# Performance work log

Measured on AMD Instinct MI355X. Metric: run time of the kernel, lower is better.

The kernel has to match this reference:

```python
import jax, jax.numpy as jnp
import numpy as np

LORA_ALPHA = 16.0
MAX_RANK = 32.0
SCALING = LORA_ALPHA / MAX_RANK  # use_rslora=False path


def setup_inputs() -> dict:
    key = jax.random.key(0)
    ks = jax.random.split(key, 9)
    d = 4096
    x = jax.random.normal(ks[0], (4, 2048, d), dtype=jnp.float32)
    W_base = jax.random.normal(ks[1], (d, d), dtype=jnp.float32) / np.sqrt(d)
    A8 = jax.random.normal(ks[2], (8, d), dtype=jnp.float32) / np.sqrt(d)
    B8 = jax.random.normal(ks[3], (d, 8), dtype=jnp.float32) * 0.01
    A16 = jax.random.normal(ks[4], (16, d), dtype=jnp.float32) / np.sqrt(d)
    B16 = jax.random.normal(ks[5], (d, 16), dtype=jnp.float32) * 0.01
    A32 = jax.random.normal(ks[6], (32, d), dtype=jnp.float32) / np.sqrt(d)
    B32 = jax.random.normal(ks[7], (d, 32), dtype=jnp.float32) * 0.01
    alphas = jax.random.normal(ks[8], (3,), dtype=jnp.float32)
    return {"x": x, "W_base": W_base, "A8": A8, "B8": B8, "A16": A16,
            "B16": B16, "A32": A32, "B32": B32, "alphas": alphas}


def reference(x, W_base, A8, B8, A16, B16, A32, B32, alphas):
    # Base layer: y = x @ W_base^T (nn.Linear, no bias)
    base = jnp.einsum('bsd,od->bso', x, W_base)
    adapter = jnp.zeros_like(base)
    for i, (A, B) in enumerate([(A8, B8), (A16, B16), (A32, B32)]):
        # lora_B(lora_A(x)): (x @ A^T) @ B^T, skinny rank-r GEMMs
        low = jnp.einsum('bsd,rd->bsr', x, A)
        out = jnp.einsum('bsr,dr->bsd', low, B)
        adapter = adapter + alphas[i] * out
    return base + adapter * SCALING
```

## Files before the change

kernel.cpp:

```cpp
#include <hip/hip_runtime.h>
#include <hip/hip_bf16.h>


typedef __attribute__((ext_vector_type(8))) short bf16x8;
typedef __attribute__((ext_vector_type(4))) float f32x4;
typedef __attribute__((ext_vector_type(8))) unsigned short u16x8;

#define GLOBAL_LOAD_LDS16(gp, lp)                                                   \
  __builtin_amdgcn_global_load_lds(                                                 \
      (const __attribute__((address_space(1))) unsigned int*)(gp),                  \
      (__attribute__((address_space(3))) unsigned int*)(lp), 16, 0, 0)

__device__ inline unsigned short bf16_rne(float f) {
  unsigned int u = __builtin_bit_cast(unsigned int, f);
  u += 0x7fffu + ((u >> 16) & 1u);
  return (unsigned short)(u >> 16);
}
__device__ inline float bf16_to_f(unsigned short h) {
  unsigned int u = ((unsigned int)h) << 16;
  return __builtin_bit_cast(float, u);
}

__global__ __launch_bounds__(256) void split_x(const float* __restrict__ x,
                                               unsigned short* __restrict__ xh,
                                               unsigned short* __restrict__ xl) {
  size_t i = ((size_t)blockIdx.x * 256 + threadIdx.x) * 8;
  float4 v0 = *(const float4*)(x + i);
  float4 v1 = *(const float4*)(x + i + 4);
  float f[8] = {v0.x, v0.y, v0.z, v0.w, v1.x, v1.y, v1.z, v1.w};
  u16x8 vh, vl;
#pragma unroll
  for (int j = 0; j < 8; ++j) {
    unsigned short h = bf16_rne(f[j]);
    vh[j] = h;
    vl[j] = bf16_rne(f[j] - bf16_to_f(h));
  }
  *(u16x8*)(xh + i) = vh;
  *(u16x8*)(xl + i) = vl;
}

__global__ __launch_bounds__(256) void fold_w(
    const float* __restrict__ W, const float* __restrict__ A8,
    const float* __restrict__ B8, const float* __restrict__ A16,
    const float* __restrict__ B16, const float* __restrict__ A32,
    const float* __restrict__ B32, const float* __restrict__ alphas,
    unsigned short* __restrict__ Wh, unsigned short* __restrict__ Wl) {
  __shared__ float Bc[16][56];
  const int tid = threadIdx.x;
  const int o0 = blockIdx.x * 16;
  const float c0 = 0.5f * alphas[0], c1 = 0.5f * alphas[1], c2 = 0.5f * alphas[2];
  for (int t = tid; t < 16 * 56; t += 256) {
    int oi = t / 56, r = t % 56, o = o0 + oi;
    float v;
    if (r < 8)
      v = c0 * B8[o * 8 + r];
    else if (r < 24)
      v = c1 * B16[o * 16 + (r - 8)];
    else
      v = c2 * B32[o * 32 + (r - 24)];
    Bc[oi][r] = v;
  }
  __syncthreads();
  for (int c = 0; c < 16; ++c) {
    const int d = c * 256 + tid;
    float a[56];
#pragma unroll
    for (int r = 0; r < 8; ++r) a[r] = A8[r * 4096 + d];
#pragma unroll
    for (int r = 0; r < 16; ++r) a[8 + r] = A16[r * 4096 + d];
#pragma unroll
    for (int r = 0; r < 32; ++r) a[24 + r] = A32[r * 4096 + d];
#pragma unroll 4
    for (int oi = 0; oi < 16; ++oi) {
      float w = W[(size_t)(o0 + oi) * 4096 + d];
#pragma unroll
      for (int r = 0; r < 56; ++r) w = fmaf(Bc[oi][r], a[r], w);
      unsigned short h = bf16_rne(w);
      Wh[(size_t)(o0 + oi) * 4096 + d] = h;
      Wl[(size_t)(o0 + oi) * 4096 + d] = bf16_rne(w - bf16_to_f(h));
    }
  }
}

__global__ __launch_bounds__(256, 3) void gemm3(const unsigned short* __restrict__ Xh,
                                                const unsigned short* __restrict__ Xl,
                                                const unsigned short* __restrict__ Wh,
                                                const unsigned short* __restrict__ Wl,
                                                float* __restrict__ C) {
  __shared__ __align__(16) unsigned short As[128 * 64];
  __shared__ __align__(16) unsigned short Bs[128 * 64];

  const int tid = threadIdx.x;
  const int lane = tid & 63;
  const int wid = tid >> 6;
  const int wm = wid >> 1, wn = wid & 1;
  const int m0 = blockIdx.y * 128;
  const int n0 = blockIdx.x * 128;

  const int srow_base = wid * 32 + (lane >> 3);
  const int lslot = (lane & 7) ^ (lane >> 3);

  f32x4 acc[4][4];
#pragma unroll
  for (int mi = 0; mi < 4; ++mi)
#pragma unroll
    for (int ni = 0; ni < 4; ++ni) acc[mi][ni] = (f32x4){0.f, 0.f, 0.f, 0.f};

  for (int pass = 0; pass < 3; ++pass) {
    const unsigned short* Ap = (pass == 2) ? Xl : Xh;
    const unsigned short* Bp = (pass == 1) ? Wl : Wh;
    for (int kt = 0; kt < 64; ++kt) {
      const int k0 = kt * 64;
      __syncthreads();
#pragma unroll
      for (int j = 0; j < 4; ++j) {
        const int row = srow_base + j * 8;
        const size_t ga = (size_t)(m0 + row) * 4096 + k0 + lslot * 8;
        GLOBAL_LOAD_LDS16(Ap + ga, (char*)As + wid * 4096 + j * 1024);
        const size_t gb = (size_t)(n0 + row) * 4096 + k0 + lslot * 8;
        GLOBAL_LOAD_LDS16(Bp + gb, (char*)Bs + wid * 4096 + j * 1024);
      }
      __syncthreads();
#pragma unroll
      for (int ks = 0; ks < 2; ++ks) {
        const int kk = ks * 32 + (lane >> 4) * 8;
        bf16x8 a[4], b[4];
#pragma unroll
        for (int mi = 0; mi < 4; ++mi) {
          const int row = wm * 64 + mi * 16 + (lane & 15);
          a[mi] = *(const bf16x8*)&As[row * 64 + (kk ^ ((row & 7) << 3))];
        }
#pragma unroll
        for (int ni = 0; ni < 4; ++ni) {
          const int row = wn * 64 + ni * 16 + (lane & 15);
          b[ni] = *(const bf16x8*)&Bs[row * 64 + (kk ^ ((row & 7) << 3))];
        }
#pragma unroll
        for (int mi = 0; mi < 4; ++mi)
#pragma unroll
          for (int ni = 0; ni < 4; ++ni)
            acc[mi][ni] = __builtin_amdgcn_mfma_f32_16x16x32_bf16(a[mi], b[ni],
                                                                  acc[mi][ni], 0, 0, 0);
      }
    }
  }

#pragma unroll
  for (int mi = 0; mi < 4; ++mi)
#pragma unroll
    for (int ni = 0; ni < 4; ++ni) {
      const int row = m0 + wm * 64 + mi * 16 + (lane >> 4) * 4;
      const int col = n0 + wn * 64 + ni * 16 + (lane & 15);
      float* cp = C + (size_t)row * 4096 + col;
      cp[0] = acc[mi][ni][0];
      cp[4096] = acc[mi][ni][1];
      cp[2 * 4096] = acc[mi][ni][2];
      cp[3 * 4096] = acc[mi][ni][3];
    }
}

extern "C" void kernel_launch(void* const* d_in, const int* in_sizes, int n_in,
                              void* d_out, int out_size, void* d_ws, size_t ws_size,
                              hipStream_t stream) {
  const float* x = (const float*)d_in[0];
  const float* Wb = (const float*)d_in[1];
  const float* A8 = (const float*)d_in[2];
  const float* B8 = (const float*)d_in[3];
  const float* A16 = (const float*)d_in[4];
  const float* B16 = (const float*)d_in[5];
  const float* A32 = (const float*)d_in[6];
  const float* B32 = (const float*)d_in[7];
  const float* al = (const float*)d_in[8];
  float* out = (float*)d_out;

  char* ws = (char*)d_ws;
  unsigned short* xh = (unsigned short*)(ws);
  unsigned short* xl = (unsigned short*)(ws + 67108864);
  unsigned short* wh = (unsigned short*)(ws + 134217728);
  unsigned short* wl = (unsigned short*)(ws + 167772160);

  split_x<<<16384, 256, 0, stream>>>(x, xh, xl);
  fold_w<<<256, 256, 0, stream>>>(Wb, A8, B8, A16, B16, A32, B32, al, wh, wl);
  gemm3<<<dim3(32, 64), 256, 0, stream>>>(xh, xl, wh, wl, out);
}
```

Measured before the change: 1.171 ms.

## Replace 3-pass GEMM with 256x256 8-wave double-buffered phased MFMA kernel

```diff
diff --git a/kernel.cpp b/kernel.cpp
--- a/kernel.cpp
+++ b/kernel.cpp
@@ -48,6 +48,7 @@
   __shared__ float Bc[16][56];
   const int tid = threadIdx.x;
   const int o0 = blockIdx.x * 16;
+  const int d0 = blockIdx.y * 2048;
   const float c0 = 0.5f * alphas[0], c1 = 0.5f * alphas[1], c2 = 0.5f * alphas[2];
   for (int t = tid; t < 16 * 56; t += 256) {
     int oi = t / 56, r = t % 56, o = o0 + oi;
@@ -61,8 +62,8 @@
     Bc[oi][r] = v;
   }
   __syncthreads();
-  for (int c = 0; c < 16; ++c) {
-    const int d = c * 256 + tid;
+  for (int c = 0; c < 8; ++c) {
+    const int d = d0 + c * 256 + tid;
     float a[56];
 #pragma unroll
     for (int r = 0; r < 8; ++r) a[r] = A8[r * 4096 + d];
@@ -82,74 +83,151 @@
   }
 }
 
-__global__ __launch_bounds__(256, 3) void gemm3(const unsigned short* __restrict__ Xh,
-                                                const unsigned short* __restrict__ Xl,
-                                                const unsigned short* __restrict__ Wh,
-                                                const unsigned short* __restrict__ Wl,
-                                                float* __restrict__ C) {
-  __shared__ __align__(16) unsigned short As[128 * 64];
-  __shared__ __align__(16) unsigned short Bs[128 * 64];
+
+#define BAR __builtin_amdgcn_s_barrier()
+#define P1 __builtin_amdgcn_s_setprio(1)
+#define P0 __builtin_amdgcn_s_setprio(0)
+#define SCHB __builtin_amdgcn_sched_barrier(0)
+#define LGKM(N) asm volatile("s_waitcnt lgkmcnt(" #N ")" ::: "memory")
+#define VMC(N) asm volatile("s_waitcnt vmcnt(" #N ")" ::: "memory")
+
+__global__ __launch_bounds__(512) void gemm8ph(const unsigned short* __restrict__ Xh,
+                                               const unsigned short* __restrict__ Xl,
+                                               const unsigned short* __restrict__ Wh,
+                                               const unsigned short* __restrict__ Wl,
+                                               float* __restrict__ C) {
+  __shared__ __align__(16) unsigned short lds[65536];
 
   const int tid = threadIdx.x;
   const int lane = tid & 63;
   const int wid = tid >> 6;
-  const int wm = wid >> 1, wn = wid & 1;
-  const int m0 = blockIdx.y * 128;
-  const int n0 = blockIdx.x * 128;
-
-  const int srow_base = wid * 32 + (lane >> 3);
-  const int lslot = (lane & 7) ^ (lane >> 3);
-
-  f32x4 acc[4][4];
-#pragma unroll
-  for (int mi = 0; mi < 4; ++mi)
+  const int wm = wid >> 2, wn = wid & 3;
+
+  const int bid = blockIdx.x;
+  const int swz = (bid & 7) * 64 + (bid >> 3);
+  const int m0 = (swz >> 4) * 256;
+  const int n0 = (swz & 15) * 256;
+
+  const int r8 = lane >> 3;
+  const int lsl = (lane & 7) ^ r8;
+  const size_t sA = (size_t)(m0 + wid * 8 + r8) * 4096 + (size_t)lsl * 8;
+  const size_t sB = (size_t)(n0 + wid * 8 + r8) * 4096 + (size_t)lsl * 8;
+
+  const int aB = wm * 8192 + (lane & 15) * 64;
+  const int bB = 16384 + (wn >> 1) * 8192 + (wn & 1) * 4096 + (lane & 15) * 64;
+  int colS[2];
+#pragma unroll
+  for (int ks = 0; ks < 2; ++ks)
+    colS[ks] = (ks * 32 + ((lane >> 4) * 8)) ^ ((lane & 7) << 3);
+
+#define LDA(BUF, MI, KS) (*(const bf16x8*)&lds[((BUF) << 15) + aB + ((MI) << 10) + colS[KS]])
+#define LDB(BUF, NI, KS) (*(const bf16x8*)&lds[((BUF) << 15) + bB + ((NI) << 10) + colS[KS]])
+
+#define STG(MAT, T, H)                                                                   \
+  do {                                                                                   \
+    const unsigned short* __restrict__ gp =                                              \
+        (MAT) ? (((unsigned)((T)-64) < 64u) ? Wl : Wh) : (((T) >= 128) ? Xl : Xh);       \
+    const size_t go = ((MAT) ? sB : sA) + (size_t)(H)*524288 + (size_t)(((T)&63) * 64);  \
+    unsigned short* lp = &lds[(((T)&1) << 15) + ((MAT) << 14) + ((H) << 13) + (wid << 9)]; \
+    GLOBAL_LOAD_LDS16(gp + go, lp);                                                      \
+    GLOBAL_LOAD_LDS16(gp + go + 262144, lp + 4096);                                      \
+  } while (0)
+
+  bf16x8 af[8][2];
+  bf16x8 bf_[4][2];
+  f32x4 acc[8][4];
+#pragma unroll
+  for (int mi = 0; mi < 8; ++mi)
 #pragma unroll
     for (int ni = 0; ni < 4; ++ni) acc[mi][ni] = (f32x4){0.f, 0.f, 0.f, 0.f};
 
-  for (int pass = 0; pass < 3; ++pass) {
-    const unsigned short* Ap = (pass == 2) ? Xl : Xh;
-    const unsigned short* Bp = (pass == 1) ? Wl : Wh;
-    for (int kt = 0; kt < 64; ++kt) {
-      const int k0 = kt * 64;
-      __syncthreads();
-#pragma unroll
-      for (int j = 0; j < 4; ++j) {
-        const int row = srow_base + j * 8;
-        const size_t ga = (size_t)(m0 + row) * 4096 + k0 + lslot * 8;
-        GLOBAL_LOAD_LDS16(Ap + ga, (char*)As + wid * 4096 + j * 1024);
-        const size_t gb = (size_t)(n0 + row) * 4096 + k0 + lslot * 8;
-        GLOBAL_LOAD_LDS16(Bp + gb, (char*)Bs + wid * 4096 + j * 1024);
-      }
-      __syncthreads();
-#pragma unroll
-      for (int ks = 0; ks < 2; ++ks) {
-        const int kk = ks * 32 + (lane >> 4) * 8;
-        bf16x8 a[4], b[4];
-#pragma unroll
-        for (int mi = 0; mi < 4; ++mi) {
-          const int row = wm * 64 + mi * 16 + (lane & 15);
-          a[mi] = *(const bf16x8*)&As[row * 64 + (kk ^ ((row & 7) << 3))];
-        }
-#pragma unroll
-        for (int ni = 0; ni < 4; ++ni) {
-          const int row = wn * 64 + ni * 16 + (lane & 15);
-          b[ni] = *(const bf16x8*)&Bs[row * 64 + (kk ^ ((row & 7) << 3))];
-        }
-#pragma unroll
-        for (int mi = 0; mi < 4; ++mi)
-#pragma unroll
-          for (int ni = 0; ni < 4; ++ni)
-            acc[mi][ni] = __builtin_amdgcn_mfma_f32_16x16x32_bf16(a[mi], b[ni],
-                                                                  acc[mi][ni], 0, 0, 0);
-      }
-    }
-  }
-
-#pragma unroll
-  for (int mi = 0; mi < 4; ++mi)
+#define RD_Q1(BUF)                                                \
+  do {                                                            \
+    _Pragma("unroll") for (int q = 0; q < 4; ++q)                 \
+        _Pragma("unroll") for (int ks = 0; ks < 2; ++ks)          \
+            af[q][ks] = LDA(BUF, q, ks);                          \
+    _Pragma("unroll") for (int q = 0; q < 2; ++q)                 \
+        _Pragma("unroll") for (int ks = 0; ks < 2; ++ks)          \
+            bf_[q][ks] = LDB(BUF, q, ks);                         \
+  } while (0)
+#define RD_Q2(BUF)                                                \
+  do {                                                            \
+    _Pragma("unroll") for (int q = 2; q < 4; ++q)                 \
+        _Pragma("unroll") for (int ks = 0; ks < 2; ++ks)          \
+            bf_[q][ks] = LDB(BUF, q, ks);                         \
+  } while (0)
+#define RD_Q3(BUF)                                                \
+  do {                                                            \
+    _Pragma("unroll") for (int q = 4; q < 8; ++q)                 \
+        _Pragma("unroll") for (int ks = 0; ks < 2; ++ks)          \
+            af[q][ks] = LDA(BUF, q, ks);                          \
+  } while (0)
+
+#define MFMAQ(MQ, NQ)                                                                    \
+  do {                                                                                   \
+    _Pragma("unroll") for (int mi = (MQ)*4; mi < (MQ)*4 + 4; ++mi)                       \
+        _Pragma("unroll") for (int ni = (NQ)*2; ni < (NQ)*2 + 2; ++ni)                   \
+            _Pragma("unroll") for (int ks = 0; ks < 2; ++ks)                             \
+                acc[mi][ni] = __builtin_amdgcn_mfma_f32_16x16x32_bf16(                   \
+                    af[mi][ks], bf_[ni][ks], acc[mi][ni], 0, 0, 0);                      \
+  } while (0)
+
+  STG(0, 0, 0);
+  STG(0, 0, 1);
+  STG(1, 0, 0);
+  STG(1, 0, 1);
+  STG(1, 1, 0);
+  STG(0, 1, 0);
+  VMC(4);
+  BAR;
+  RD_Q1(0);
+
+#pragma clang loop unroll(disable)
+  for (int it = 0; it < 95; ++it) {
+    const int O = 2 * it + 1, E2 = 2 * it + 2, O2 = 2 * it + 3;
+    RD_Q2(0);
+    STG(1, O, 1);
+    BAR; LGKM(4); SCHB; P1; MFMAQ(0, 0); P0; BAR;
+    RD_Q3(0);
+    STG(0, O, 1);
+    BAR; LGKM(8); SCHB; P1; MFMAQ(0, 1); P0; BAR;
+    STG(1, E2, 0);
+    BAR; LGKM(0); SCHB; P1; MFMAQ(1, 0); P0; VMC(2); BAR;
+    RD_Q1(1);
+    STG(0, E2, 0);
+    BAR; LGKM(12); SCHB; P1; MFMAQ(1, 1); P0; BAR;
+    RD_Q2(1);
+    STG(1, E2, 1);
+    BAR; LGKM(4); SCHB; P1; MFMAQ(0, 0); P0; BAR;
+    RD_Q3(1);
+    STG(0, E2, 1);
+    BAR; LGKM(8); SCHB; P1; MFMAQ(0, 1); P0; BAR;
+    STG(1, O2, 0);
+    BAR; LGKM(0); SCHB; P1; MFMAQ(1, 0); P0; VMC(2); BAR;
+    RD_Q1(0);
+    STG(0, O2, 0);
+    BAR; LGKM(12); SCHB; P1; MFMAQ(1, 1); P0; BAR;
+  }
+
+  RD_Q2(0); STG(1, 191, 1);
+  BAR; LGKM(4); SCHB; P1; MFMAQ(0, 0); P0; BAR;
+  RD_Q3(0); STG(0, 191, 1);
+  BAR; LGKM(8); SCHB; P1; MFMAQ(0, 1); P0; BAR;
+  BAR; LGKM(0); SCHB; P1; MFMAQ(1, 0); P0; VMC(0); BAR;
+  RD_Q1(1);
+  BAR; LGKM(12); SCHB; P1; MFMAQ(1, 1); P0; BAR;
+  RD_Q2(1);
+  BAR; LGKM(4); SCHB; P1; MFMAQ(0, 0); P0; BAR;
+  RD_Q3(1);
+  BAR; LGKM(8); SCHB; P1; MFMAQ(0, 1); P0; BAR;
+  BAR; LGKM(0); SCHB; P1; MFMAQ(1, 0); P0; BAR;
+  LGKM(0); P1; MFMAQ(1, 1); P0;
+
+#pragma unroll
+  for (int mi = 0; mi < 8; ++mi)
 #pragma unroll
     for (int ni = 0; ni < 4; ++ni) {
-      const int row = m0 + wm * 64 + mi * 16 + (lane >> 4) * 4;
+      const int row = m0 + wm * 128 + mi * 16 + (lane >> 4) * 4;
       const int col = n0 + wn * 64 + ni * 16 + (lane & 15);
       float* cp = C + (size_t)row * 4096 + col;
       cp[0] = acc[mi][ni][0];
@@ -180,6 +258,6 @@
   unsigned short* wl = (unsigned short*)(ws + 167772160);
 
   split_x<<<16384, 256, 0, stream>>>(x, xh, xl);
-  fold_w<<<256, 256, 0, stream>>>(Wb, A8, B8, A16, B16, A32, B32, al, wh, wl);
-  gemm3<<<dim3(32, 64), 256, 0, stream>>>(xh, xl, wh, wl, out);
-}
+  fold_w<<<dim3(256, 2), 256, 0, stream>>>(Wb, A8, B8, A16, B16, A32, B32, al, wh, wl);
+  gemm8ph<<<512, 512, 0, stream>>>(xh, xl, wh, wl, out);
+}
```

New measurement: 2.200 ms. +87.9%, slower.
